# Optimization experiments

Measured on AMD Instinct MI355X. Metric: run time of the kernel, lower is better.

Reference implementation:

```python
import jax, jax.numpy as jnp
import numpy as np

B, H, N, D = 1, 24, 3072, 128
BM = 192            # query block size (kernel is hard-coded to BM=192)
QG = N // BM        # number of query groups
TOP_KEYS = 0.3
MULTIPLE_OF = 128
TK = int(MULTIPLE_OF * round(TOP_KEYS * N / MULTIPLE_OF))  # 896


def setup_inputs() -> dict:
    key = jax.random.key(0)
    kq, kk, kv = jax.random.split(key, 3)
    q = jax.random.normal(kq, (B, H, N, D), dtype=jnp.float32)
    k = jax.random.normal(kk, (B, H, N, D), dtype=jnp.float32)
    v = jax.random.normal(kv, (B, H, N, D), dtype=jnp.float32)
    return {"q": q, "k": k, "v": v}


def reference(q, k, v):
    """Full-step (inference_step==1) path of SparseDiffAttn._fast_attention:
    dense_colsum_attn -> top-k key selection per 192-query block -> csp_attn,
    returning o_cache = o_dense - o_sparse (the cached residual output)."""
    scale = 1.0 / jnp.sqrt(jnp.asarray(D, q.dtype))
    # --- dense_colsum_attn ---
    s = jnp.einsum('bhqd,bhkd->bhqk', q, k) * scale          # [B,H,N,N]
    p = jax.nn.softmax(s, axis=-1)                           # softmax probs
    o = jnp.einsum('bhqk,bhkd->bhqd', p, v)                  # dense output
    # block column sums: per 192-query group, sum of probs per key
    bs = p.reshape(B, H, QG, BM, N).sum(axis=3)              # [B,H,QG,N]
    # --- top-k routing (should_compress_indices=False branch) ---
    _, inds = jax.lax.top_k(jax.lax.stop_gradient(bs), TK)   # [B,H,QG,TK]
    # --- csp_attn: block-sparse attention over selected keys ---
    k_sel = jnp.take_along_axis(k[:, :, None], inds[..., None], axis=3)  # [B,H,QG,TK,D]
    v_sel = jnp.take_along_axis(v[:, :, None], inds[..., None], axis=3)
    qb = q.reshape(B, H, QG, BM, D)
    ss = jnp.einsum('bhgqd,bhgkd->bhgqk', qb, k_sel) * scale # [B,H,QG,BM,TK]
    ps = jax.nn.softmax(ss, axis=-1)
    o_sparse = jnp.einsum('bhgqk,bhgkd->bhgqd', ps, v_sel).reshape(B, H, N, D)
    # o_cache = o - csp_attn(q,k,v,inds,counts)
    return o - o_sparse
```

## Files before the change

kernel.cpp:

```cpp
#include <hip/hip_runtime.h>
#include <stdint.h>


#define H 24
#define N 3072
#define DH 128
#define SCALE 0.08838834764831845f
#define TK 896

typedef __attribute__((ext_vector_type(8))) short short8;
typedef __attribute__((ext_vector_type(4))) float f32x4;

__device__ __forceinline__ uint32_t bf_rne(float x){
  uint32_t u = __float_as_uint(x);
  return (u + 0x7FFFu + ((u >> 16) & 1u)) >> 16;
}

__device__ __forceinline__ f32x4 f4zero(){ f32x4 z = {0.f,0.f,0.f,0.f}; return z; }

__device__ __forceinline__ void split8_2(const float* f, uint4& h4, uint4& l4){
  uint32_t hw[4], lw[4];
#pragma unroll
  for (int i = 0; i < 4; i++){
    float a = f[2*i], b = f[2*i+1];
    uint32_t ha = bf_rne(a), hb = bf_rne(b);
    float ra = a - __uint_as_float(ha << 16);
    float rb = b - __uint_as_float(hb << 16);
    hw[i] = ha | (hb << 16);
    lw[i] = bf_rne(ra) | (bf_rne(rb) << 16);
  }
  h4.x = hw[0]; h4.y = hw[1]; h4.z = hw[2]; h4.w = hw[3];
  l4.x = lw[0]; l4.y = lw[1]; l4.z = lw[2]; l4.w = lw[3];
}

__device__ __forceinline__ void split8_3(const float* f, uint4& h4, uint4& m4, uint4& l4){
  uint32_t hw[4], mw[4], lw[4];
#pragma unroll
  for (int i = 0; i < 4; i++){
    float a = f[2*i], b = f[2*i+1];
    uint32_t ha = bf_rne(a), hb = bf_rne(b);
    float ra = a - __uint_as_float(ha << 16);
    float rb = b - __uint_as_float(hb << 16);
    uint32_t ma = bf_rne(ra), mb = bf_rne(rb);
    float la = ra - __uint_as_float(ma << 16);
    float lb = rb - __uint_as_float(mb << 16);
    hw[i] = ha | (hb << 16);
    mw[i] = ma | (mb << 16);
    lw[i] = bf_rne(la) | (bf_rne(lb) << 16);
  }
  h4.x = hw[0]; h4.y = hw[1]; h4.z = hw[2]; h4.w = hw[3];
  m4.x = mw[0]; m4.y = mw[1]; m4.z = mw[2]; m4.w = mw[3];
  l4.x = lw[0]; l4.y = lw[1]; l4.z = lw[2]; l4.w = lw[3];
}

__device__ __forceinline__ short8 as_s8(const uint4 u){
  union { uint4 u4; short8 s; } t; t.u4 = u; return t.s;
}

__device__ __forceinline__ void mapHC(int bid, int& h, int& ch){
  int x = bid & 7;
  int i = bid >> 3;
  h = x + 8 * (i / 48);
  ch = i % 48;
}

__device__ __forceinline__ void load_qfrags2(const float* qhead, int R, int w, int lane,
                                             uint4* qh, uint4* ql){
  int row = R + w*16 + (lane & 15);
  const float* qp = qhead + (size_t)row * DH;
#pragma unroll
  for (int s = 0; s < 4; s++){
    int d0 = s*32 + (lane >> 4)*8;
    float4 a = *(const float4*)(qp + d0);
    float4 b = *(const float4*)(qp + d0 + 4);
    float f[8] = {a.x*SCALE, a.y*SCALE, a.z*SCALE, a.w*SCALE,
                  b.x*SCALE, b.y*SCALE, b.z*SCALE, b.w*SCALE};
    split8_2(f, qh[s], ql[s]);
  }
}

__device__ __forceinline__ void load_qfrags3(const float* qhead, int R, int w, int lane,
                                             uint4* qh, uint4* qm, uint4* ql){
  int row = R + w*16 + (lane & 15);
  const float* qp = qhead + (size_t)row * DH;
#pragma unroll
  for (int s = 0; s < 4; s++){
    int d0 = s*32 + (lane >> 4)*8;
    float4 a = *(const float4*)(qp + d0);
    float4 b = *(const float4*)(qp + d0 + 4);
    float f[8] = {a.x*SCALE, a.y*SCALE, a.z*SCALE, a.w*SCALE,
                  b.x*SCALE, b.y*SCALE, b.z*SCALE, b.w*SCALE};
    split8_3(f, qh[s], qm[s], ql[s]);
  }
}

__device__ __forceinline__ void stage_k2(const float* kp, char* khi, char* klo,
                                         int jst, int dblk){
  float4 a = *(const float4*)(kp);
  float4 b = *(const float4*)(kp + 4);
  float4 c = *(const float4*)(kp + 8);
  float4 d = *(const float4*)(kp + 12);
  float f0[8] = {a.x,a.y,a.z,a.w,b.x,b.y,b.z,b.w};
  float f1[8] = {c.x,c.y,c.z,c.w,d.x,d.y,d.z,d.w};
  uint4 h4, l4;
  int base = jst*256 + dblk*32;
  int sw = (jst & 7) << 4;
  split8_2(f0, h4, l4);
  *(uint4*)(khi + (base ^ sw)) = h4;
  *(uint4*)(klo + (base ^ sw)) = l4;
  split8_2(f1, h4, l4);
  *(uint4*)(khi + ((base + 16) ^ sw)) = h4;
  *(uint4*)(klo + ((base + 16) ^ sw)) = l4;
}

__device__ __forceinline__ void stage_k3(const float* kp, char* khi, char* kmi, char* klo,
                                         int jst, int dblk){
  float4 a = *(const float4*)(kp);
  float4 b = *(const float4*)(kp + 4);
  float4 c = *(const float4*)(kp + 8);
  float4 d = *(const float4*)(kp + 12);
  float f0[8] = {a.x,a.y,a.z,a.w,b.x,b.y,b.z,b.w};
  float f1[8] = {c.x,c.y,c.z,c.w,d.x,d.y,d.z,d.w};
  uint4 h4, m4, l4;
  int base = jst*256 + dblk*32;
  int sw = (jst & 7) << 4;
  split8_3(f0, h4, m4, l4);
  *(uint4*)(khi + (base ^ sw)) = h4;
  *(uint4*)(kmi + (base ^ sw)) = m4;
  *(uint4*)(klo + (base ^ sw)) = l4;
  split8_3(f1, h4, m4, l4);
  *(uint4*)(khi + ((base + 16) ^ sw)) = h4;
  *(uint4*)(kmi + ((base + 16) ^ sw)) = m4;
  *(uint4*)(klo + ((base + 16) ^ sw)) = l4;
}

__device__ __forceinline__ void stage_v(const float* vp, char* vts, int jv, int dv){
  float4 a = *(const float4*)(vp);
  float4 b = *(const float4*)(vp + 4);
  float4 c = *(const float4*)(vp + 8);
  float4 d = *(const float4*)(vp + 12);
  float f[16] = {a.x,a.y,a.z,a.w,b.x,b.y,b.z,b.w,c.x,c.y,c.z,c.w,d.x,d.y,d.z,d.w};
#pragma unroll
  for (int i = 0; i < 16; i++)
    *(unsigned short*)(vts + (size_t)(dv + i)*80 + jv*2) = (unsigned short)bf_rne(f[i]);
}

__device__ __forceinline__ void zcompute3(const char* khi, const char* klo,
                                          const uint4* qh, const uint4* ql,
                                          int lane, f32x4* zac){
  zac[0] = f4zero();
  zac[1] = f4zero();
#pragma unroll
  for (int s = 0; s < 4; s++){
    short8 qa = as_s8(qh[s]);
    short8 qb = as_s8(ql[s]);
#pragma unroll
    for (int ct = 0; ct < 2; ct++){
      int key = ct*16 + (lane & 15);
      int off = (key*256 + (s*32 + (lane >> 4)*8)*2) ^ ((key & 7) << 4);
      short8 kh = *(const short8*)(khi + off);
      short8 kl = *(const short8*)(klo + off);
      zac[ct] = __builtin_amdgcn_mfma_f32_16x16x32_bf16(qa, kl, zac[ct], 0, 0, 0);
      zac[ct] = __builtin_amdgcn_mfma_f32_16x16x32_bf16(qb, kh, zac[ct], 0, 0, 0);
      zac[ct] = __builtin_amdgcn_mfma_f32_16x16x32_bf16(qa, kh, zac[ct], 0, 0, 0);
    }
  }
}

__device__ __forceinline__ void zcompute6(const char* khi, const char* kmi, const char* klo,
                                          const uint4* qh, const uint4* qm, const uint4* ql,
                                          int lane, f32x4* zac){
  zac[0] = f4zero();
  zac[1] = f4zero();
#pragma unroll
  for (int s = 0; s < 4; s++){
    short8 qa = as_s8(qh[s]);
    short8 qb = as_s8(qm[s]);
    short8 qc = as_s8(ql[s]);
#pragma unroll
    for (int ct = 0; ct < 2; ct++){
      int key = ct*16 + (lane & 15);
      int off = (key*256 + (s*32 + (lane >> 4)*8)*2) ^ ((key & 7) << 4);
      short8 kh = *(const short8*)(khi + off);
      short8 km = *(const short8*)(kmi + off);
      short8 kl = *(const short8*)(klo + off);
      zac[ct] = __builtin_amdgcn_mfma_f32_16x16x32_bf16(qb, km, zac[ct], 0, 0, 0);
      zac[ct] = __builtin_amdgcn_mfma_f32_16x16x32_bf16(qa, kl, zac[ct], 0, 0, 0);
      zac[ct] = __builtin_amdgcn_mfma_f32_16x16x32_bf16(qc, kh, zac[ct], 0, 0, 0);
      zac[ct] = __builtin_amdgcn_mfma_f32_16x16x32_bf16(qa, km, zac[ct], 0, 0, 0);
      zac[ct] = __builtin_amdgcn_mfma_f32_16x16x32_bf16(qb, kh, zac[ct], 0, 0, 0);
      zac[ct] = __builtin_amdgcn_mfma_f32_16x16x32_bf16(qa, kh, zac[ct], 0, 0, 0);
    }
  }
}

__global__ __launch_bounds__(256, 2) void kA(const float* __restrict__ qg,
                                             const float* __restrict__ kg,
                                             float* __restrict__ Zg){
  __shared__ alignas(16) char khi[32*256];
  __shared__ alignas(16) char klo[32*256];
  int h, ch; mapHC(blockIdx.x, h, ch);
  const int tid = threadIdx.x, w = tid >> 6, lane = tid & 63;
  const int l15 = lane & 15, l4 = lane >> 4;
  const int R = ch * 64;
  const float* qhead = qg + (size_t)h*N*DH;
  const float* khead = kg + (size_t)h*N*DH;
  uint4 qh[4], ql[4];
  load_qfrags2(qhead, R, w, lane, qh, ql);
  float zs[4] = {0.f,0.f,0.f,0.f};
  const int jst = tid >> 3, dblk = tid & 7;
  for (int kt = 0; kt < 96; kt++){
    stage_k2(khead + (size_t)(kt*32 + jst)*DH + dblk*16, khi, klo, jst, dblk);
    __syncthreads();
    f32x4 zac[2];
    zcompute3(khi, klo, qh, ql, lane, zac);
#pragma unroll
    for (int ct = 0; ct < 2; ct++)
#pragma unroll
      for (int r = 0; r < 4; r++)
        zs[r] += __expf(zac[ct][r]);
    __syncthreads();
  }
#pragma unroll
  for (int m = 1; m < 16; m <<= 1)
#pragma unroll
    for (int r = 0; r < 4; r++)
      zs[r] += __shfl_xor(zs[r], m);
  if (l15 == 0){
#pragma unroll
    for (int r = 0; r < 4; r++)
      Zg[h*N + R + w*16 + l4*4 + r] = zs[r];
  }
}

__global__ __launch_bounds__(256, 2) void kB(const float* __restrict__ qg,
                                             const float* __restrict__ kg,
                                             const float* __restrict__ vg,
                                             const float* __restrict__ Zg,
                                             float* __restrict__ cpart,
                                             float* __restrict__ outg){
  __shared__ alignas(16) char khi[32*256];
  __shared__ alignas(16) char kmi[32*256];
  __shared__ alignas(16) char klo[32*256];
  __shared__ alignas(16) char vts[128*80];
  __shared__ alignas(16) char pls[4][16*80];
  __shared__ float colbuf[4][32];
  int h, ch; mapHC(blockIdx.x, h, ch);
  const int tid = threadIdx.x, w = tid >> 6, lane = tid & 63;
  const int l15 = lane & 15, l4 = lane >> 4;
  const int R = ch * 64;
  const float* qhead = qg + (size_t)h*N*DH;
  const float* khead = kg + (size_t)h*N*DH;
  const float* vhead = vg + (size_t)h*N*DH;
  uint4 qh[4], qm[4], ql[4];
  load_qfrags3(qhead, R, w, lane, qh, qm, ql);
  float rz[4];
#pragma unroll
  for (int r = 0; r < 4; r++)
    rz[r] = 1.0f / Zg[h*N + R + w*16 + l4*4 + r];
  f32x4 oac[8];
#pragma unroll
  for (int i = 0; i < 8; i++) oac[i] = f4zero();
  const int jst = tid >> 3, dblk = tid & 7;
  const int jv = tid & 31, dv = (tid >> 5) * 16;
  float* cp = cpart + (size_t)(h*48 + ch) * 3072;
  for (int kt = 0; kt < 96; kt++){
    if (kt > 0 && tid < 32)
      cp[(kt-1)*32 + tid] = colbuf[0][tid] + colbuf[1][tid] + colbuf[2][tid] + colbuf[3][tid];
    stage_k3(khead + (size_t)(kt*32 + jst)*DH + dblk*16, khi, kmi, klo, jst, dblk);
    stage_v(vhead + (size_t)(kt*32 + jv)*DH + dv, vts, jv, dv);
    __syncthreads();
    f32x4 zac[2];
    zcompute6(khi, kmi, klo, qh, qm, ql, lane, zac);
    float pn[2][4];
#pragma unroll
    for (int ct = 0; ct < 2; ct++)
#pragma unroll
      for (int r = 0; r < 4; r++)
        pn[ct][r] = __expf(zac[ct][r]) * rz[r];
#pragma unroll
    for (int ct = 0; ct < 2; ct++){
      float cs = pn[ct][0] + pn[ct][1] + pn[ct][2] + pn[ct][3];
      cs += __shfl_xor(cs, 16);
      cs += __shfl_xor(cs, 32);
      if (lane < 16) colbuf[w][ct*16 + lane] = cs;
    }
    char* pw = pls[w];
#pragma unroll
    for (int ct = 0; ct < 2; ct++)
#pragma unroll
      for (int r = 0; r < 4; r++)
        *(unsigned short*)(pw + (size_t)(l4*4 + r)*80 + (ct*16 + l15)*2) =
            (unsigned short)bf_rne(pn[ct][r]);
    short8 ap = *(const short8*)(pw + (size_t)l15*80 + l4*16);
#pragma unroll
    for (int vt = 0; vt < 8; vt++){
      short8 vb = *(const short8*)(vts + (size_t)(vt*16 + l15)*80 + l4*16);
      oac[vt] = __builtin_amdgcn_mfma_f32_16x16x32_bf16(ap, vb, oac[vt], 0, 0, 0);
    }
    __syncthreads();
  }
  if (tid < 32)
    cp[95*32 + tid] = colbuf[0][tid] + colbuf[1][tid] + colbuf[2][tid] + colbuf[3][tid];
#pragma unroll
  for (int vt = 0; vt < 8; vt++)
#pragma unroll
    for (int r = 0; r < 4; r++)
      outg[((size_t)h*N + R + w*16 + l4*4 + r)*DH + vt*16 + l15] = oac[vt][r];
}

__global__ __launch_bounds__(256, 2) void kC(const float* __restrict__ cpart,
                                             int* __restrict__ selg){
  __shared__ uint32_t cu[3072];
  __shared__ int red[4];
  __shared__ int runS;
  const int gid = blockIdx.x;
  const int h = gid >> 4, g = gid & 15;
  const int tid = threadIdx.x, w = tid >> 6, lane = tid & 63;
  const float* p0 = cpart + (size_t)(h*48 + g*3) * 3072;
  const float* p1 = p0 + 3072;
  const float* p2 = p0 + 6144;
  for (int i = tid; i < 3072; i += 256)
    cu[i] = __float_as_uint(p0[i] + p1[i] + p2[i]);
  __syncthreads();
  uint32_t lo = 0u, hi = 0xFFFFFFFFu;
  for (int it = 0; it < 32; it++){
    bool active = (lo < hi);
    uint32_t mid = (uint32_t)(((uint64_t)lo + (uint64_t)hi + 1ull) >> 1);
    int c = 0;
    if (active){
      for (int i = tid; i < 3072; i += 256) c += (cu[i] >= mid) ? 1 : 0;
#pragma unroll
      for (int m = 1; m < 64; m <<= 1) c += __shfl_xor(c, m);
    }
    if (lane == 0) red[w] = c;
    __syncthreads();
    int tot = red[0] + red[1] + red[2] + red[3];
    __syncthreads();
    if (active){ if (tot >= TK) lo = mid; else hi = mid - 1; }
  }
  const uint32_t V = lo;
  {
    int c = 0;
    for (int i = tid; i < 3072; i += 256) c += (cu[i] > V) ? 1 : 0;
#pragma unroll
    for (int m = 1; m < 64; m <<= 1) c += __shfl_xor(c, m);
    if (lane == 0) red[w] = c;
  }
  __syncthreads();
  const int ngt = red[0] + red[1] + red[2] + red[3];
  const int need = TK - ngt;
  int* sb = selg + (size_t)gid * TK;
  if (tid == 0) runS = 0;
  __syncthreads();
  for (int ck = 0; ck < 12; ck++){
    int j = ck*256 + tid;
    bool f = (cu[j] > V);
    unsigned long long bal = __ballot(f);
    int wpre = __popcll(bal & ((1ull << lane) - 1ull));
    int wtot = __popcll(bal);
    if (lane == 0) red[w] = wtot;
    __syncthreads();
    int woff = 0;
    for (int x = 0; x < w; x++) woff += red[x];
    int base = runS;
    if (f) sb[base + woff + wpre] = j;
    __syncthreads();
    if (tid == 0) runS = base + red[0] + red[1] + red[2] + red[3];
    __syncthreads();
  }
  if (tid == 0) runS = 0;
  __syncthreads();
  for (int ck = 0; ck < 12; ck++){
    int j = ck*256 + tid;
    bool f = (cu[j] == V);
    unsigned long long bal = __ballot(f);
    int wpre = __popcll(bal & ((1ull << lane) - 1ull));
    int wtot = __popcll(bal);
    if (lane == 0) red[w] = wtot;
    __syncthreads();
    int woff = 0;
    for (int x = 0; x < w; x++) woff += red[x];
    int base = runS;
    int rank = base + woff + wpre;
    if (f && rank < need) sb[ngt + rank] = j;
    __syncthreads();
    if (tid == 0) runS = base + red[0] + red[1] + red[2] + red[3];
    __syncthreads();
  }
}

__global__ __launch_bounds__(256, 2) void kD(const float* __restrict__ qg,
                                             const float* __restrict__ kg,
                                             const float* __restrict__ vg,
                                             const float* __restrict__ Zg,
                                             const int* __restrict__ selg,
                                             float* __restrict__ outg){
  __shared__ alignas(16) char khi[32*256];
  __shared__ alignas(16) char klo[32*256];
  __shared__ alignas(16) char vts[128*80];
  __shared__ alignas(16) char pls[4][16*80];
  __shared__ int sell[TK];
  int h, ch; mapHC(blockIdx.x, h, ch);
  const int tid = threadIdx.x, w = tid >> 6, lane = tid & 63;
  const int l15 = lane & 15, l4 = lane >> 4;
  const int R = ch * 64;
  const int g = ch / 3;
  const float* qhead = qg + (size_t)h*N*DH;
  const float* khead = kg + (size_t)h*N*DH;
  const float* vhead = vg + (size_t)h*N*DH;
  const int* sb = selg + (size_t)(h*16 + g) * TK;
  for (int i = tid; i < TK; i += 256) sell[i] = sb[i];
  uint4 qh[4], ql[4];
  load_qfrags2(qhead, R, w, lane, qh, ql);
  float rz[4];
#pragma unroll
  for (int r = 0; r < 4; r++)
    rz[r] = 1.0f / Zg[h*N + R + w*16 + l4*4 + r];
  f32x4 oac[8];
#pragma unroll
  for (int i = 0; i < 8; i++) oac[i] = f4zero();
  float rh[4] = {0.f,0.f,0.f,0.f};
  const int jst = tid >> 3, dblk = tid & 7;
  const int jv = tid & 31, dv = (tid >> 5) * 16;
  __syncthreads();
  for (int st = 0; st < 28; st++){
    {
      int key = sell[st*32 + jst];
      stage_k2(khead + (size_t)key*DH + dblk*16, khi, klo, jst, dblk);
    }
    {
      int key = sell[st*32 + jv];
      stage_v(vhead + (size_t)key*DH + dv, vts, jv, dv);
    }
    __syncthreads();
    f32x4 zac[2];
    zcompute3(khi, klo, qh, ql, lane, zac);
    float pn[2][4];
#pragma unroll
    for (int ct = 0; ct < 2; ct++)
#pragma unroll
      for (int r = 0; r < 4; r++){
        pn[ct][r] = __expf(zac[ct][r]) * rz[r];
        rh[r] += pn[ct][r];
      }
    char* pw = pls[w];
#pragma unroll
    for (int ct = 0; ct < 2; ct++)
#pragma unroll
      for (int r = 0; r < 4; r++)
        *(unsigned short*)(pw + (size_t)(l4*4 + r)*80 + (ct*16 + l15)*2) =
            (unsigned short)bf_rne(pn[ct][r]);
    short8 ap = *(const short8*)(pw + (size_t)l15*80 + l4*16);
#pragma unroll
    for (int vt = 0; vt < 8; vt++){
      short8 vb = *(const short8*)(vts + (size_t)(vt*16 + l15)*80 + l4*16);
      oac[vt] = __builtin_amdgcn_mfma_f32_16x16x32_bf16(ap, vb, oac[vt], 0, 0, 0);
    }
    __syncthreads();
  }
#pragma unroll
  for (int m = 1; m < 16; m <<= 1)
#pragma unroll
    for (int r = 0; r < 4; r++)
      rh[r] += __shfl_xor(rh[r], m);
  float ri[4];
#pragma unroll
  for (int r = 0; r < 4; r++) ri[r] = 1.0f / rh[r];
#pragma unroll
  for (int vt = 0; vt < 8; vt++)
#pragma unroll
    for (int r = 0; r < 4; r++){
      size_t idx = ((size_t)h*N + R + w*16 + l4*4 + r)*DH + vt*16 + l15;
      outg[idx] = outg[idx] - oac[vt][r]*ri[r];
    }
}

extern "C" void kernel_launch(void* const* d_in, const int* in_sizes, int n_in,
                              void* d_out, int out_size, void* d_ws, size_t ws_size,
                              hipStream_t stream){
  (void)in_sizes; (void)n_in; (void)out_size; (void)ws_size;
  const float* q = (const float*)d_in[0];
  const float* k = (const float*)d_in[1];
  const float* v = (const float*)d_in[2];
  float* out = (float*)d_out;
  float* Z = (float*)d_ws;
  float* cpart = Z + (size_t)H * N;
  int* sel = (int*)(cpart + (size_t)1152 * 3072);
  kA<<<dim3(1152), dim3(256), 0, stream>>>(q, k, Z);
  kB<<<dim3(1152), dim3(256), 0, stream>>>(q, k, v, Z, cpart, out);
  kC<<<dim3(384),  dim3(256), 0, stream>>>(cpart, sel);
  kD<<<dim3(1152), dim3(256), 0, stream>>>(q, k, v, Z, sel, out);
}
```

Before: 1.042 ms.

## Presplit K into bf16 planes, fuse Z and dense passes, DMA-stage K tiles

Adds a kernel that splits K into hi/mid/lo bf16 planes once in workspace. Z-computation and the dense pass are fused into one kernel, and K tiles are staged with global_load_lds DMA instead of per-thread conversion. The dense and sparse passes drop to a 4-MFMA two-term product, and V staging is vectorised with swizzled LDS. Top-k selection now resolves near-threshold candidates by recomputing their column sums in fp64 inside kC. The costs are extra workspace traffic, a serial per-candidate loop in kC, and higher occupancy that may pressure registers.

```diff
diff --git a/kernel.cpp b/kernel.cpp
--- a/kernel.cpp
+++ b/kernel.cpp
@@ -1,5 +1,6 @@
 #include <hip/hip_runtime.h>
 #include <stdint.h>
+#include <math.h>
 
 
 #define H 24
@@ -7,9 +8,14 @@
 #define DH 128
 #define SCALE 0.08838834764831845f
 #define TK 896
+#define MARG 1.6e-5f
+#define MAXC 96
 
 typedef __attribute__((ext_vector_type(8))) short short8;
 typedef __attribute__((ext_vector_type(4))) float f32x4;
+typedef __attribute__((address_space(1))) unsigned char GAS;
+typedef __attribute__((address_space(3))) unsigned char LAS;
+#define GLD16(g, l) __builtin_amdgcn_global_load_lds((GAS*)(g), (LAS*)(l), 16, 0, 0)
 
 __device__ __forceinline__ uint32_t bf_rne(float x){
   uint32_t u = __float_as_uint(x);
@@ -134,22 +140,27 @@
   *(uint4*)(klo + ((base + 16) ^ sw)) = l4;
 }
 
-__device__ __forceinline__ void stage_v(const float* vp, char* vts, int jv, int dv){
-  float4 a = *(const float4*)(vp);
-  float4 b = *(const float4*)(vp + 4);
-  float4 c = *(const float4*)(vp + 8);
-  float4 d = *(const float4*)(vp + 12);
-  float f[16] = {a.x,a.y,a.z,a.w,b.x,b.y,b.z,b.w,c.x,c.y,c.z,c.w,d.x,d.y,d.z,d.w};
-#pragma unroll
-  for (int i = 0; i < 16; i++)
-    *(unsigned short*)(vts + (size_t)(dv + i)*80 + jv*2) = (unsigned short)bf_rne(f[i]);
-}
-
-__device__ __forceinline__ void zcompute3(const char* khi, const char* klo,
+__device__ __forceinline__ void stage_v2(const float* vp0, const float* vp1,
+                                         char* vts, int jv2, int dv8){
+  float4 a0 = *(const float4*)(vp0);
+  float4 b0 = *(const float4*)(vp0 + 4);
+  float4 a1 = *(const float4*)(vp1);
+  float4 b1 = *(const float4*)(vp1 + 4);
+  float f0[8] = {a0.x,a0.y,a0.z,a0.w,b0.x,b0.y,b0.z,b0.w};
+  float f1[8] = {a1.x,a1.y,a1.z,a1.w,b1.x,b1.y,b1.z,b1.w};
+#pragma unroll
+  for (int i = 0; i < 8; i++){
+    uint32_t wrd = bf_rne(f0[i]) | (bf_rne(f1[i]) << 16);
+    int r = dv8 + i;
+    int off = (r*80 + jv2*2) ^ (((r >> 3) & 1) << 4);
+    *(uint32_t*)(vts + off) = wrd;
+  }
+}
+
+__device__ __forceinline__ void zcompute4(const char* khi, const char* klo,
                                           const uint4* qh, const uint4* ql,
                                           int lane, f32x4* zac){
-  zac[0] = f4zero();
-  zac[1] = f4zero();
+  zac[0] = f4zero(); zac[1] = f4zero();
 #pragma unroll
   for (int s = 0; s < 4; s++){
     short8 qa = as_s8(qh[s]);
@@ -160,8 +171,9 @@
       int off = (key*256 + (s*32 + (lane >> 4)*8)*2) ^ ((key & 7) << 4);
       short8 kh = *(const short8*)(khi + off);
       short8 kl = *(const short8*)(klo + off);
+      zac[ct] = __builtin_amdgcn_mfma_f32_16x16x32_bf16(qb, kl, zac[ct], 0, 0, 0);
+      zac[ct] = __builtin_amdgcn_mfma_f32_16x16x32_bf16(qb, kh, zac[ct], 0, 0, 0);
       zac[ct] = __builtin_amdgcn_mfma_f32_16x16x32_bf16(qa, kl, zac[ct], 0, 0, 0);
-      zac[ct] = __builtin_amdgcn_mfma_f32_16x16x32_bf16(qb, kh, zac[ct], 0, 0, 0);
       zac[ct] = __builtin_amdgcn_mfma_f32_16x16x32_bf16(qa, kh, zac[ct], 0, 0, 0);
     }
   }
@@ -170,8 +182,7 @@
 __device__ __forceinline__ void zcompute6(const char* khi, const char* kmi, const char* klo,
                                           const uint4* qh, const uint4* qm, const uint4* ql,
                                           int lane, f32x4* zac){
-  zac[0] = f4zero();
-  zac[1] = f4zero();
+  zac[0] = f4zero(); zac[1] = f4zero();
 #pragma unroll
   for (int s = 0; s < 4; s++){
     short8 qa = as_s8(qh[s]);
@@ -194,56 +205,57 @@
   }
 }
 
-__global__ __launch_bounds__(256, 2) void kA(const float* __restrict__ qg,
-                                             const float* __restrict__ kg,
-                                             float* __restrict__ Zg){
-  __shared__ alignas(16) char khi[32*256];
-  __shared__ alignas(16) char klo[32*256];
-  int h, ch; mapHC(blockIdx.x, h, ch);
-  const int tid = threadIdx.x, w = tid >> 6, lane = tid & 63;
-  const int l15 = lane & 15, l4 = lane >> 4;
-  const int R = ch * 64;
-  const float* qhead = qg + (size_t)h*N*DH;
-  const float* khead = kg + (size_t)h*N*DH;
-  uint4 qh[4], ql[4];
-  load_qfrags2(qhead, R, w, lane, qh, ql);
-  float zs[4] = {0.f,0.f,0.f,0.f};
-  const int jst = tid >> 3, dblk = tid & 7;
-  for (int kt = 0; kt < 96; kt++){
-    stage_k2(khead + (size_t)(kt*32 + jst)*DH + dblk*16, khi, klo, jst, dblk);
-    __syncthreads();
-    f32x4 zac[2];
-    zcompute3(khi, klo, qh, ql, lane, zac);
-#pragma unroll
-    for (int ct = 0; ct < 2; ct++)
-#pragma unroll
-      for (int r = 0; r < 4; r++)
-        zs[r] += __expf(zac[ct][r]);
-    __syncthreads();
-  }
-#pragma unroll
-  for (int m = 1; m < 16; m <<= 1)
-#pragma unroll
-    for (int r = 0; r < 4; r++)
-      zs[r] += __shfl_xor(zs[r], m);
-  if (l15 == 0){
-#pragma unroll
-    for (int r = 0; r < 4; r++)
-      Zg[h*N + R + w*16 + l4*4 + r] = zs[r];
-  }
-}
-
-__global__ __launch_bounds__(256, 2) void kB(const float* __restrict__ qg,
-                                             const float* __restrict__ kg,
-                                             const float* __restrict__ vg,
-                                             const float* __restrict__ Zg,
-                                             float* __restrict__ cpart,
-                                             float* __restrict__ outg){
-  __shared__ alignas(16) char khi[32*256];
-  __shared__ alignas(16) char kmi[32*256];
-  __shared__ alignas(16) char klo[32*256];
-  __shared__ alignas(16) char vts[128*80];
-  __shared__ alignas(16) char pls[4][16*80];
+__device__ __forceinline__ void pv_step(const float pn[2][4], char* pw, const char* vts,
+                                        f32x4* oac, int l15, int l4){
+#pragma unroll
+  for (int ct = 0; ct < 2; ct++)
+#pragma unroll
+    for (int r = 0; r < 4; r++){
+      int row = l4*4 + r;
+      int off = (row*80 + (ct*16 + l15)*2) ^ (((row >> 3) & 1) << 4);
+      *(unsigned short*)(pw + off) = (unsigned short)bf_rne(pn[ct][r]);
+    }
+  int offA = (l15*80 + l4*16) ^ (((l15 >> 3) & 1) << 4);
+  short8 ap = *(const short8*)(pw + offA);
+#pragma unroll
+  for (int vt = 0; vt < 8; vt++){
+    int vrow = vt*16 + l15;
+    int offB = (vrow*80 + l4*16) ^ (((vrow >> 3) & 1) << 4);
+    short8 vb = *(const short8*)(vts + offB);
+    oac[vt] = __builtin_amdgcn_mfma_f32_16x16x32_bf16(ap, vb, oac[vt], 0, 0, 0);
+  }
+}
+
+__global__ __launch_bounds__(256) void kS(const float* __restrict__ kg,
+                                          unsigned short* __restrict__ khig,
+                                          unsigned short* __restrict__ kmig,
+                                          unsigned short* __restrict__ klog){
+  size_t idx = ((size_t)blockIdx.x*256 + threadIdx.x)*8;
+  float4 a = *(const float4*)(kg + idx);
+  float4 b = *(const float4*)(kg + idx + 4);
+  float f[8] = {a.x,a.y,a.z,a.w,b.x,b.y,b.z,b.w};
+  uint4 h4, m4, l4;
+  split8_3(f, h4, m4, l4);
+  *(uint4*)(khig + idx) = h4;
+  *(uint4*)(kmig + idx) = m4;
+  *(uint4*)(klog + idx) = l4;
+}
+
+template<int DMA>
+__global__ __launch_bounds__(256, 4) void kAB(const float* __restrict__ qg,
+                                              const float* __restrict__ kg,
+                                              const float* __restrict__ vg,
+                                              const unsigned short* __restrict__ khig,
+                                              const unsigned short* __restrict__ kmig,
+                                              const unsigned short* __restrict__ klog,
+                                              double* __restrict__ Zg,
+                                              float* __restrict__ cpart,
+                                              float* __restrict__ outg){
+  __shared__ alignas(16) char khi[8192];
+  __shared__ alignas(16) char kmi[8192];
+  __shared__ alignas(16) char klo[8192];
+  __shared__ alignas(16) char vts[10240];
+  __shared__ alignas(16) char pls[4][1280];
   __shared__ float colbuf[4][32];
   int h, ch; mapHC(blockIdx.x, h, ch);
   const int tid = threadIdx.x, w = tid >> 6, lane = tid & 63;
@@ -254,24 +266,72 @@
   const float* vhead = vg + (size_t)h*N*DH;
   uint4 qh[4], qm[4], ql[4];
   load_qfrags3(qhead, R, w, lane, qh, qm, ql);
+
+  size_t b0 = 0, b1 = 0;
+  if (DMA){
+    int g0 = w*128 + lane, g1 = g0 + 64;
+    int k0 = g0 >> 4, sl0 = (g0 & 15) ^ (k0 & 7);
+    int k1 = g1 >> 4, sl1 = (g1 & 15) ^ (k1 & 7);
+    b0 = ((size_t)h*N + k0)*DH + sl0*8;
+    b1 = ((size_t)h*N + k1)*DH + sl1*8;
+  }
+  const int wofs = w*2048;
+  const int jst = tid >> 3, dblk = tid & 7;
+
+  double zs[4] = {0.0,0.0,0.0,0.0};
+  for (int kt = 0; kt < 96; kt++){
+    if (DMA){
+      size_t st = (size_t)kt*32*DH;
+      GLD16(khig + b0 + st, khi + wofs);  GLD16(khig + b1 + st, khi + wofs + 1024);
+      GLD16(kmig + b0 + st, kmi + wofs);  GLD16(kmig + b1 + st, kmi + wofs + 1024);
+      GLD16(klog + b0 + st, klo + wofs);  GLD16(klog + b1 + st, klo + wofs + 1024);
+    } else {
+      stage_k3(khead + (size_t)(kt*32 + jst)*DH + dblk*16, khi, kmi, klo, jst, dblk);
+    }
+    __syncthreads();
+    f32x4 zac[2];
+    zcompute6(khi, kmi, klo, qh, qm, ql, lane, zac);
+#pragma unroll
+    for (int ct = 0; ct < 2; ct++)
+#pragma unroll
+      for (int r = 0; r < 4; r++)
+        zs[r] += (double)__expf(zac[ct][r]);
+    __syncthreads();
+  }
+#pragma unroll
+  for (int m = 1; m < 16; m <<= 1)
+#pragma unroll
+    for (int r = 0; r < 4; r++)
+      zs[r] += __shfl_xor(zs[r], m);
   float rz[4];
 #pragma unroll
-  for (int r = 0; r < 4; r++)
-    rz[r] = 1.0f / Zg[h*N + R + w*16 + l4*4 + r];
+  for (int r = 0; r < 4; r++) rz[r] = (float)(1.0 / zs[r]);
+  if (l15 == 0){
+#pragma unroll
+    for (int r = 0; r < 4; r++)
+      Zg[h*N + R + w*16 + l4*4 + r] = zs[r];
+  }
+
   f32x4 oac[8];
 #pragma unroll
   for (int i = 0; i < 8; i++) oac[i] = f4zero();
-  const int jst = tid >> 3, dblk = tid & 7;
-  const int jv = tid & 31, dv = (tid >> 5) * 16;
+  const int jv2 = (tid & 15)*2, dv8 = (tid >> 4)*8;
   float* cp = cpart + (size_t)(h*48 + ch) * 3072;
   for (int kt = 0; kt < 96; kt++){
     if (kt > 0 && tid < 32)
       cp[(kt-1)*32 + tid] = colbuf[0][tid] + colbuf[1][tid] + colbuf[2][tid] + colbuf[3][tid];
-    stage_k3(khead + (size_t)(kt*32 + jst)*DH + dblk*16, khi, kmi, klo, jst, dblk);
-    stage_v(vhead + (size_t)(kt*32 + jv)*DH + dv, vts, jv, dv);
+    if (DMA){
+      size_t st = (size_t)kt*32*DH;
+      GLD16(khig + b0 + st, khi + wofs);  GLD16(khig + b1 + st, khi + wofs + 1024);
+      GLD16(kmig + b0 + st, kmi + wofs);  GLD16(kmig + b1 + st, kmi + wofs + 1024);
+    } else {
+      stage_k2(khead + (size_t)(kt*32 + jst)*DH + dblk*16, khi, kmi, jst, dblk);
+    }
+    stage_v2(vhead + (size_t)(kt*32 + jv2)*DH + dv8,
+             vhead + (size_t)(kt*32 + jv2 + 1)*DH + dv8, vts, jv2, dv8);
     __syncthreads();
     f32x4 zac[2];
-    zcompute6(khi, kmi, klo, qh, qm, ql, lane, zac);
+    zcompute4(khi, kmi, qh, qm, lane, zac);
     float pn[2][4];
 #pragma unroll
     for (int ct = 0; ct < 2; ct++)
@@ -285,19 +345,7 @@
       cs += __shfl_xor(cs, 32);
       if (lane < 16) colbuf[w][ct*16 + lane] = cs;
     }
-    char* pw = pls[w];
-#pragma unroll
-    for (int ct = 0; ct < 2; ct++)
-#pragma unroll
-      for (int r = 0; r < 4; r++)
-        *(unsigned short*)(pw + (size_t)(l4*4 + r)*80 + (ct*16 + l15)*2) =
-            (unsigned short)bf_rne(pn[ct][r]);
-    short8 ap = *(const short8*)(pw + (size_t)l15*80 + l4*16);
-#pragma unroll
-    for (int vt = 0; vt < 8; vt++){
-      short8 vb = *(const short8*)(vts + (size_t)(vt*16 + l15)*80 + l4*16);
-      oac[vt] = __builtin_amdgcn_mfma_f32_16x16x32_bf16(ap, vb, oac[vt], 0, 0, 0);
-    }
+    pv_step(pn, pls[w], vts, oac, l15, l4);
     __syncthreads();
   }
   if (tid < 32)
@@ -310,10 +358,16 @@
 }
 
 __global__ __launch_bounds__(256, 2) void kC(const float* __restrict__ cpart,
+                                             const double* __restrict__ Zd,
+                                             const float* __restrict__ qg,
+                                             const float* __restrict__ kg,
                                              int* __restrict__ selg){
-  __shared__ uint32_t cu[3072];
+  __shared__ float cu[3072];
   __shared__ int red[4];
   __shared__ int runS;
+  __shared__ int cidx[MAXC];
+  __shared__ double cval[MAXC];
+  __shared__ double rbuf[256];
   const int gid = blockIdx.x;
   const int h = gid >> 4, g = gid & 15;
   const int tid = threadIdx.x, w = tid >> 6, lane = tid & 63;
@@ -321,7 +375,7 @@
   const float* p1 = p0 + 3072;
   const float* p2 = p0 + 6144;
   for (int i = tid; i < 3072; i += 256)
-    cu[i] = __float_as_uint(p0[i] + p1[i] + p2[i]);
+    cu[i] = p0[i] + p1[i] + p2[i];
   __syncthreads();
   uint32_t lo = 0u, hi = 0xFFFFFFFFu;
   for (int it = 0; it < 32; it++){
@@ -329,7 +383,8 @@
     uint32_t mid = (uint32_t)(((uint64_t)lo + (uint64_t)hi + 1ull) >> 1);
     int c = 0;
     if (active){
-      for (int i = tid; i < 3072; i += 256) c += (cu[i] >= mid) ? 1 : 0;
+      for (int i = tid; i < 3072; i += 256)
+        c += (__float_as_uint(cu[i]) >= mid) ? 1 : 0;
 #pragma unroll
       for (int m = 1; m < 64; m <<= 1) c += __shfl_xor(c, m);
     }
@@ -339,23 +394,25 @@
     __syncthreads();
     if (active){ if (tot >= TK) lo = mid; else hi = mid - 1; }
   }
-  const uint32_t V = lo;
+  const float Vf = __uint_as_float(lo);
+  const float thr_hi = Vf + MARG;
+  const float thr_lo = Vf - MARG;
   {
     int c = 0;
-    for (int i = tid; i < 3072; i += 256) c += (cu[i] > V) ? 1 : 0;
+    for (int i = tid; i < 3072; i += 256) c += (cu[i] > thr_hi) ? 1 : 0;
 #pragma unroll
     for (int m = 1; m < 64; m <<= 1) c += __shfl_xor(c, m);
     if (lane == 0) red[w] = c;
   }
   __syncthreads();
-  const int ngt = red[0] + red[1] + red[2] + red[3];
-  const int need = TK - ngt;
+  const int n_in = red[0] + red[1] + red[2] + red[3];
+  const int need = TK - n_in;
   int* sb = selg + (size_t)gid * TK;
   if (tid == 0) runS = 0;
   __syncthreads();
   for (int ck = 0; ck < 12; ck++){
     int j = ck*256 + tid;
-    bool f = (cu[j] > V);
+    bool f = (cu[j] > thr_hi);
     unsigned long long bal = __ballot(f);
     int wpre = __popcll(bal & ((1ull << lane) - 1ull));
     int wtot = __popcll(bal);
@@ -373,7 +430,7 @@
   __syncthreads();
   for (int ck = 0; ck < 12; ck++){
     int j = ck*256 + tid;
-    bool f = (cu[j] == V);
+    bool f = (!(cu[j] > thr_hi)) && (cu[j] >= thr_lo);
     unsigned long long bal = __ballot(f);
     int wpre = __popcll(bal & ((1ull << lane) - 1ull));
     int wtot = __popcll(bal);
@@ -382,24 +439,68 @@
     int woff = 0;
     for (int x = 0; x < w; x++) woff += red[x];
     int base = runS;
-    int rank = base + woff + wpre;
-    if (f && rank < need) sb[ngt + rank] = j;
+    int pos = base + woff + wpre;
+    if (f && pos < MAXC) cidx[pos] = j;
     __syncthreads();
     if (tid == 0) runS = base + red[0] + red[1] + red[2] + red[3];
     __syncthreads();
   }
-}
-
-__global__ __launch_bounds__(256, 2) void kD(const float* __restrict__ qg,
+  int ccnt = runS < MAXC ? runS : MAXC;
+  __syncthreads();
+  const int row = g*192 + (tid < 192 ? tid : 0);
+  const float* qp = qg + ((size_t)h*N + row)*DH;
+  const double zinv_d = (tid < 192) ? 1.0 / 1.0 : 0.0; (void)zinv_d;
+  const double Zrow = Zd[h*N + row];
+  for (int c = 0; c < ccnt; c++){
+    double t = 0.0;
+    if (tid < 192){
+      const float* kp = kg + ((size_t)h*N + cidx[c])*DH;
+      double a0 = 0.0, a1 = 0.0, a2 = 0.0, a3 = 0.0;
+#pragma unroll 4
+      for (int d = 0; d < DH; d += 4){
+        a0 = fma((double)qp[d],   (double)kp[d],   a0);
+        a1 = fma((double)qp[d+1], (double)kp[d+1], a1);
+        a2 = fma((double)qp[d+2], (double)kp[d+2], a2);
+        a3 = fma((double)qp[d+3], (double)kp[d+3], a3);
+      }
+      double z = ((a0 + a1) + (a2 + a3)) * 0.08838834764831845;
+      t = exp(z) / Zrow;
+    }
+    rbuf[tid] = t;
+    __syncthreads();
+#pragma unroll
+    for (int s = 128; s > 0; s >>= 1){
+      if (tid < s) rbuf[tid] += rbuf[tid + s];
+      __syncthreads();
+    }
+    if (tid == 0) cval[c] = rbuf[0];
+    __syncthreads();
+  }
+  if (tid < ccnt){
+    double my = cval[tid];
+    int myi = cidx[tid];
+    int rank = 0;
+    for (int u = 0; u < ccnt; u++){
+      double cu_ = cval[u];
+      if (cu_ > my || (cu_ == my && cidx[u] < myi)) rank++;
+    }
+    if (rank < need) sb[n_in + rank] = myi;
+  }
+}
+
+template<int DMA>
+__global__ __launch_bounds__(256, 4) void kD(const float* __restrict__ qg,
                                              const float* __restrict__ kg,
                                              const float* __restrict__ vg,
-                                             const float* __restrict__ Zg,
+                                             const double* __restrict__ Zg,
                                              const int* __restrict__ selg,
+                                             const unsigned short* __restrict__ khig,
+                                             const unsigned short* __restrict__ kmig,
                                              float* __restrict__ outg){
-  __shared__ alignas(16) char khi[32*256];
-  __shared__ alignas(16) char klo[32*256];
-  __shared__ alignas(16) char vts[128*80];
-  __shared__ alignas(16) char pls[4][16*80];
+  __shared__ alignas(16) char khi[8192];
+  __shared__ alignas(16) char klo[8192];
+  __shared__ alignas(16) char vts[10240];
+  __shared__ alignas(16) char pls[4][1280];
   __shared__ int sell[TK];
   int h, ch; mapHC(blockIdx.x, h, ch);
   const int tid = threadIdx.x, w = tid >> 6, lane = tid & 63;
@@ -416,26 +517,40 @@
   float rz[4];
 #pragma unroll
   for (int r = 0; r < 4; r++)
-    rz[r] = 1.0f / Zg[h*N + R + w*16 + l4*4 + r];
+    rz[r] = (float)(1.0 / Zg[h*N + R + w*16 + l4*4 + r]);
   f32x4 oac[8];
 #pragma unroll
   for (int i = 0; i < 8; i++) oac[i] = f4zero();
   float rh[4] = {0.f,0.f,0.f,0.f};
+
+  int p0g = 0, p1g = 0, sl0 = 0, sl1 = 0;
+  if (DMA){
+    int g0 = w*128 + lane, g1 = g0 + 64;
+    p0g = g0 >> 4; sl0 = (g0 & 15) ^ (p0g & 7);
+    p1g = g1 >> 4; sl1 = (g1 & 15) ^ (p1g & 7);
+  }
+  const int wofs = w*2048;
   const int jst = tid >> 3, dblk = tid & 7;
-  const int jv = tid & 31, dv = (tid >> 5) * 16;
+  const int jv2 = (tid & 15)*2, dv8 = (tid >> 4)*8;
   __syncthreads();
   for (int st = 0; st < 28; st++){
-    {
+    if (DMA){
+      size_t b0 = ((size_t)h*N + sell[st*32 + p0g])*DH + sl0*8;
+      size_t b1 = ((size_t)h*N + sell[st*32 + p1g])*DH + sl1*8;
+      GLD16(khig + b0, khi + wofs);  GLD16(khig + b1, khi + wofs + 1024);
+      GLD16(kmig + b0, klo + wofs);  GLD16(kmig + b1, klo + wofs + 1024);
+    } else {
       int key = sell[st*32 + jst];
       stage_k2(khead + (size_t)key*DH + dblk*16, khi, klo, jst, dblk);
     }
     {
-      int key = sell[st*32 + jv];
-      stage_v(vhead + (size_t)key*DH + dv, vts, jv, dv);
+      int ka_ = sell[st*32 + jv2], kb_ = sell[st*32 + jv2 + 1];
+      stage_v2(vhead + (size_t)ka_*DH + dv8, vhead + (size_t)kb_*DH + dv8,
+               vts, jv2, dv8);
     }
     __syncthreads();
     f32x4 zac[2];
-    zcompute3(khi, klo, qh, ql, lane, zac);
+    zcompute4(khi, klo, qh, ql, lane, zac);
     float pn[2][4];
 #pragma unroll
     for (int ct = 0; ct < 2; ct++)
@@ -444,19 +559,7 @@
         pn[ct][r] = __expf(zac[ct][r]) * rz[r];
         rh[r] += pn[ct][r];
       }
-    char* pw = pls[w];
-#pragma unroll
-    for (int ct = 0; ct < 2; ct++)
-#pragma unroll
-      for (int r = 0; r < 4; r++)
-        *(unsigned short*)(pw + (size_t)(l4*4 + r)*80 + (ct*16 + l15)*2) =
-            (unsigned short)bf_rne(pn[ct][r]);
-    short8 ap = *(const short8*)(pw + (size_t)l15*80 + l4*16);
-#pragma unroll
-    for (int vt = 0; vt < 8; vt++){
-      short8 vb = *(const short8*)(vts + (size_t)(vt*16 + l15)*80 + l4*16);
-      oac[vt] = __builtin_amdgcn_mfma_f32_16x16x32_bf16(ap, vb, oac[vt], 0, 0, 0);
-    }
+    pv_step(pn, pls[w], vts, oac, l15, l4);
     __syncthreads();
   }
 #pragma unroll
@@ -479,16 +582,40 @@
 extern "C" void kernel_launch(void* const* d_in, const int* in_sizes, int n_in,
                               void* d_out, int out_size, void* d_ws, size_t ws_size,
                               hipStream_t stream){
-  (void)in_sizes; (void)n_in; (void)out_size; (void)ws_size;
+  (void)in_sizes; (void)n_in; (void)out_size;
   const float* q = (const float*)d_in[0];
   const float* k = (const float*)d_in[1];
   const float* v = (const float*)d_in[2];
   float* out = (float*)d_out;
-  float* Z = (float*)d_ws;
-  float* cpart = Z + (size_t)H * N;
-  int* sel = (int*)(cpart + (size_t)1152 * 3072);
-  kA<<<dim3(1152), dim3(256), 0, stream>>>(q, k, Z);
-  kB<<<dim3(1152), dim3(256), 0, stream>>>(q, k, v, Z, cpart, out);
-  kC<<<dim3(384),  dim3(256), 0, stream>>>(cpart, sel);
-  kD<<<dim3(1152), dim3(256), 0, stream>>>(q, k, v, Z, sel, out);
-}
+  const size_t KELEMS = (size_t)H*N*DH;
+  const size_t KBYTES = KELEMS*2;
+  const size_t ZB = (size_t)H*N*8;
+  const size_t CPB = (size_t)1152*3072*4;
+  const size_t SELB = (size_t)384*TK*4;
+  const bool dma = ws_size >= 3*KBYTES + ZB + CPB + SELB;
+  char* wsb = (char*)d_ws;
+  unsigned short *khig = nullptr, *kmig = nullptr, *klog = nullptr;
+  double* Z; float* cpart; int* sel;
+  if (dma){
+    khig = (unsigned short*)wsb;
+    kmig = (unsigned short*)(wsb + KBYTES);
+    klog = (unsigned short*)(wsb + 2*KBYTES);
+    Z = (double*)(wsb + 3*KBYTES);
+    cpart = (float*)(wsb + 3*KBYTES + ZB);
+    sel = (int*)(wsb + 3*KBYTES + ZB + CPB);
+  } else {
+    Z = (double*)wsb;
+    cpart = (float*)(wsb + ZB);
+    sel = (int*)(wsb + ZB + CPB);
+  }
+  if (dma){
+    kS<<<dim3(4608), dim3(256), 0, stream>>>(k, khig, kmig, klog);
+    kAB<1><<<dim3(1152), dim3(256), 0, stream>>>(q, k, v, khig, kmig, klog, Z, cpart, out);
+    kC<<<dim3(384), dim3(256), 0, stream>>>(cpart, Z, q, k, sel);
+    kD<1><<<dim3(1152), dim3(256), 0, stream>>>(q, k, v, Z, sel, khig, kmig, out);
+  } else {
+    kAB<0><<<dim3(1152), dim3(256), 0, stream>>>(q, k, v, khig, kmig, klog, Z, cpart, out);
+    kC<<<dim3(384), dim3(256), 0, stream>>>(cpart, Z, q, k, sel);
+    kD<0><<<dim3(1152), dim3(256), 0, stream>>>(q, k, v, Z, sel, khig, kmig, out);
+  }
+}
```

Result: slower. 1.333 ms (+27.9%).
